# Kernel tuning notes

Measured on AMD Instinct MI355X. Metric: run time of the kernel, lower is better.

## Reference

```python
import jax, jax.numpy as jnp
import numpy as np

N = 8192          # number of nodes
A = 3             # number of adjacency relations
D_IN = 256
D_OUT = 64


def setup_inputs() -> dict:
    key = jax.random.key(0)
    k1, k2, k3, k4 = jax.random.split(key, 4)
    inputs = jax.random.normal(k1, (N, D_IN), dtype=jnp.float32)
    # dense adjacency stack [A, N, N] (weighted graph)
    adj_set = jax.random.uniform(k2, (A, N, N), dtype=jnp.float32)
    att = jax.random.uniform(k3, (A,), dtype=jnp.float32)
    w = jax.random.normal(k4, (D_IN, D_OUT), dtype=jnp.float32) * (1.0 / np.sqrt(D_IN))
    b = jnp.zeros((D_OUT,), dtype=jnp.float32)
    return {"inputs": inputs, "adj_set": adj_set, "att": att, "w": w, "b": b}


def reference(inputs, adj_set, att, w, b):
    # dropout=False -> identity; note: self.relu is never applied in forward
    support = jnp.matmul(inputs, w) + b                      # [N, D_OUT]
    # outputs = sum_i att[i] * (adj_i @ support), fused as one einsum
    outputs = jnp.einsum("a,anm,md->nd", att, adj_set, support)
    return outputs
```

## Files before the change

### kernel.cpp

```cpp
#include <hip/hip_runtime.h>
#include <hip/hip_bf16.h>


#define NNODES 8192
#define DIN    256
#define DOUT   64
#define NA     3
#define KSTACK (NA * NNODES)
#define KQ     (KSTACK / 4)
#define BK     256
#define NCH    (KQ / BK)
#define NSTRIP (NNODES / 64)

typedef float f32x4 __attribute__((ext_vector_type(4)));
typedef short s16x8 __attribute__((ext_vector_type(8)));

__device__ __forceinline__ unsigned short f2bf(float f) {
    __hip_bfloat16 h = __float2bfloat16(f);
    return __builtin_bit_cast(unsigned short, h);
}

__device__ __forceinline__ s16x8 pack8(f32x4 a, f32x4 b) {
    s16x8 o;
    o[0] = (short)f2bf(a[0]); o[1] = (short)f2bf(a[1]);
    o[2] = (short)f2bf(a[2]); o[3] = (short)f2bf(a[3]);
    o[4] = (short)f2bf(b[0]); o[5] = (short)f2bf(b[1]);
    o[6] = (short)f2bf(b[2]); o[7] = (short)f2bf(b[3]);
    return o;
}

__device__ __forceinline__ void gload_lds16(const float* g, float* l) {
    __builtin_amdgcn_global_load_lds(
        (const __attribute__((address_space(1))) void*)g,
        (__attribute__((address_space(3))) void*)l, 16, 0, 2);
}

__global__ __launch_bounds__(256) void zero_out(float* __restrict__ out) {
    f32x4 z = {0.f, 0.f, 0.f, 0.f};
    ((f32x4*)out)[(blockIdx.x << 8) + threadIdx.x] = z;
}

__global__ __launch_bounds__(256) void prep_support(
    const float* __restrict__ x, const float* __restrict__ w,
    const float* __restrict__ bias, const float* __restrict__ att,
    unsigned short* __restrict__ Bp)
{
    const int t = threadIdx.x;
    const int d = t & 63;
    const int m = (blockIdx.x << 2) + (t >> 6);

    const float* xr = x + (size_t)m * DIN;
    float acc = bias[d];
#pragma unroll 4
    for (int k = 0; k < DIN; k += 4) {
        f32x4 xv = *(const f32x4*)(xr + k);
        acc += xv[0] * w[(k + 0) * DOUT + d];
        acc += xv[1] * w[(k + 1) * DOUT + d];
        acc += xv[2] * w[(k + 2) * DOUT + d];
        acc += xv[3] * w[(k + 3) * DOUT + d];
    }

    const int kt   = m >> 5;
    const int kl   = m & 31;
    const int lane = ((kl >> 3) << 4) | (d & 15);
    const int j    = kl & 7;
    const int nt   = d >> 4;

    const size_t base    = (size_t)(kt * 4 + nt) * 512 + lane * 8 + j;
    const size_t aStride = (size_t)(NNODES / 32) * 4 * 512;

    const float a0 = att[0], a1 = att[1], a2 = att[2];
    Bp[base]               = f2bf(a0 * acc);
    Bp[base + aStride]     = f2bf(a1 * acc);
    Bp[base + 2 * aStride] = f2bf(a2 * acc);
}

__global__ __launch_bounds__(256, 2) void graphconv_gemm(
    const float* __restrict__ adj, const unsigned short* __restrict__ Bp,
    float* __restrict__ out)
{
    __shared__ float ldsf[16384];

    const int tid  = threadIdx.x;
    const int wv   = tid >> 6;
    const int lane = tid & 63;
    const int r    = lane & 15;
    const int g    = lane >> 4;
    const int r7   = r & 7;
    const int q     = blockIdx.x & 3;
    const int strip = blockIdx.x >> 2;
    const int row0  = strip * 64 + wv * 16;

    float* wbuf = &ldsf[wv << 12];

    f32x4 acc0 = {0.f, 0.f, 0.f, 0.f};
    f32x4 acc1 = {0.f, 0.f, 0.f, 0.f};
    f32x4 acc2 = {0.f, 0.f, 0.f, 0.f};
    f32x4 acc3 = {0.f, 0.f, 0.f, 0.f};

    const int c0 = (wv * 6 + strip) % NCH;

    for (int i = 0; i < NCH; ++i) {
        int c = c0 + i; if (c >= NCH) c -= NCH;
        const int k0 = q * KQ + c * BK;
        const float* ab = adj + ((size_t)(k0 >> 13) << 26) + (k0 & 8191);

#pragma unroll
        for (int p = 0; p < 16; ++p) {
            const float* gp = ab + (size_t)(row0 + p) * NNODES
                                 + ((lane ^ (p & 7)) << 2);
            gload_lds16(gp, wbuf + (p << 8));
        }
        asm volatile("s_waitcnt vmcnt(0)" ::: "memory");
        __builtin_amdgcn_sched_barrier(0);

        const s16x8* bp = (const s16x8*)Bp + ((size_t)(k0 >> 5) << 8) + lane;
        const float* lrow = wbuf + (r << 8);
#pragma unroll
        for (int t = 0; t < 8; ++t) {
            f32x4 v0 = *(const f32x4*)(lrow + ((t * 8 + ((2 * g) ^ r7)) << 2));
            f32x4 v1 = *(const f32x4*)(lrow + ((t * 8 + ((2 * g + 1) ^ r7)) << 2));
            s16x8 af = pack8(v0, v1);
            s16x8 b0 = bp[0];
            s16x8 b1 = bp[64];
            s16x8 b2 = bp[128];
            s16x8 b3 = bp[192];
            acc0 = __builtin_amdgcn_mfma_f32_16x16x32_bf16(af, b0, acc0, 0, 0, 0);
            acc1 = __builtin_amdgcn_mfma_f32_16x16x32_bf16(af, b1, acc1, 0, 0, 0);
            acc2 = __builtin_amdgcn_mfma_f32_16x16x32_bf16(af, b2, acc2, 0, 0, 0);
            acc3 = __builtin_amdgcn_mfma_f32_16x16x32_bf16(af, b3, acc3, 0, 0, 0);
            bp += 256;
        }
    }

    float* op = out + (size_t)row0 * DOUT;
#pragma unroll
    for (int j = 0; j < 4; ++j) {
        float* rp = op + (size_t)(4 * g + j) * DOUT + r;
        atomicAdd(rp,      acc0[j]);
        atomicAdd(rp + 16, acc1[j]);
        atomicAdd(rp + 32, acc2[j]);
        atomicAdd(rp + 48, acc3[j]);
    }
}

extern "C" void kernel_launch(void* const* d_in, const int* in_sizes, int n_in,
                              void* d_out, int out_size, void* d_ws, size_t ws_size,
                              hipStream_t stream) {
    const float* x   = (const float*)d_in[0];
    const float* adj = (const float*)d_in[1];
    const float* att = (const float*)d_in[2];
    const float* w   = (const float*)d_in[3];
    const float* b   = (const float*)d_in[4];
    float* out = (float*)d_out;
    unsigned short* Bp = (unsigned short*)d_ws;

    zero_out<<<NNODES * DOUT / 1024, 256, 0, stream>>>(out);
    prep_support<<<NNODES / 4, 256, 0, stream>>>(x, w, b, att, Bp);
    graphconv_gemm<<<NSTRIP * 4, 256, 0, stream>>>(adj, Bp, out);
}
```

Before: 186.4 us.

## Double-buffer per-wave adjacency staging and prefetch B fragments into registers

Each wave now owns two LDS buffers and issues the global-to-LDS loads for the next adjacency chunk before computing on the current one, waiting only on the older loads. All 32 B fragments for a chunk are loaded into registers up front instead of being interleaved with the MFMAs. LDS use doubles and launch bounds drop to one block per CU. This trades occupancy for explicit load/compute overlap.

```diff
diff --git a/kernel.cpp b/kernel.cpp
--- a/kernel.cpp
+++ b/kernel.cpp
@@ -75,11 +75,23 @@
     Bp[base + 2 * aStride] = f2bf(a2 * acc);
 }
 
-__global__ __launch_bounds__(256, 2) void graphconv_gemm(
+__device__ __forceinline__ void stage_chunk(
+    const float* __restrict__ adj, int row0, int k0, float* bufbase, int lane)
+{
+    const float* ab = adj + ((size_t)(k0 >> 13) << 26) + (k0 & 8191);
+#pragma unroll
+    for (int p = 0; p < 16; ++p) {
+        const float* gp = ab + (size_t)(row0 + p) * NNODES
+                             + ((lane ^ (p & 7)) << 2);
+        gload_lds16(gp, bufbase + (p << 8));
+    }
+}
+
+__global__ __launch_bounds__(256, 1) void graphconv_gemm(
     const float* __restrict__ adj, const unsigned short* __restrict__ Bp,
     float* __restrict__ out)
 {
-    __shared__ float ldsf[16384];
+    __shared__ float ldsf[32768];
 
     const int tid  = threadIdx.x;
     const int wv   = tid >> 6;
@@ -91,7 +103,7 @@
     const int strip = blockIdx.x >> 2;
     const int row0  = strip * 64 + wv * 16;
 
-    float* wbuf = &ldsf[wv << 12];
+    float* wbase = &ldsf[wv << 13];
 
     f32x4 acc0 = {0.f, 0.f, 0.f, 0.f};
     f32x4 acc1 = {0.f, 0.f, 0.f, 0.f};
@@ -100,36 +112,46 @@
 
     const int c0 = (wv * 6 + strip) % NCH;
 
+    stage_chunk(adj, row0, q * KQ + c0 * BK, wbase, lane);
+
     for (int i = 0; i < NCH; ++i) {
         int c = c0 + i; if (c >= NCH) c -= NCH;
-        const int k0 = q * KQ + c * BK;
-        const float* ab = adj + ((size_t)(k0 >> 13) << 26) + (k0 & 8191);
+        const int k0  = q * KQ + c * BK;
+        const int cur = i & 1;
 
+        const s16x8* __restrict__ bp =
+            (const s16x8*)Bp + ((size_t)(k0 >> 5) << 8) + lane;
+        s16x8 bq[32];
 #pragma unroll
-        for (int p = 0; p < 16; ++p) {
-            const float* gp = ab + (size_t)(row0 + p) * NNODES
-                                 + ((lane ^ (p & 7)) << 2);
-            gload_lds16(gp, wbuf + (p << 8));
-        }
-        asm volatile("s_waitcnt vmcnt(0)" ::: "memory");
+        for (int t = 0; t < 8; ++t)
+#pragma unroll
+            for (int n = 0; n < 4; ++n)
+                bq[t * 4 + n] = bp[t * 256 + n * 64];
+
         __builtin_amdgcn_sched_barrier(0);
 
-        const s16x8* bp = (const s16x8*)Bp + ((size_t)(k0 >> 5) << 8) + lane;
-        const float* lrow = wbuf + (r << 8);
+        const bool more = (i + 1 < NCH);
+        if (more) {
+            int cn = c + 1; if (cn >= NCH) cn = 0;
+            stage_chunk(adj, row0, q * KQ + cn * BK, wbase + ((cur ^ 1) << 12), lane);
+            asm volatile("s_waitcnt vmcnt(16)" ::: "memory");
+        } else {
+            asm volatile("s_waitcnt vmcnt(0)" ::: "memory");
+        }
+        __builtin_amdgcn_sched_barrier(0);
+
+        const float* lrow = wbase + (cur << 12) + (r << 8);
 #pragma unroll
         for (int t = 0; t < 8; ++t) {
-            f32x4 v0 = *(const f32x4*)(lrow + ((t * 8 + ((2 * g) ^ r7)) << 2));
-            f32x4 v1 = *(const f32x4*)(lrow + ((t * 8 + ((2 * g + 1) ^ r7)) << 2));
+            const int s0 = ((t << 3) + 2 * g)     ^ r7;
+            const int s1 = ((t << 3) + 2 * g + 1) ^ r7;
+            f32x4 v0 = *(const f32x4*)(lrow + (s0 << 2));
+            f32x4 v1 = *(const f32x4*)(lrow + (s1 << 2));
             s16x8 af = pack8(v0, v1);
-            s16x8 b0 = bp[0];
-            s16x8 b1 = bp[64];
-            s16x8 b2 = bp[128];
-            s16x8 b3 = bp[192];
-            acc0 = __builtin_amdgcn_mfma_f32_16x16x32_bf16(af, b0, acc0, 0, 0, 0);
-            acc1 = __builtin_amdgcn_mfma_f32_16x16x32_bf16(af, b1, acc1, 0, 0, 0);
-            acc2 = __builtin_amdgcn_mfma_f32_16x16x32_bf16(af, b2, acc2, 0, 0, 0);
-            acc3 = __builtin_amdgcn_mfma_f32_16x16x32_bf16(af, b3, acc3, 0, 0, 0);
-            bp += 256;
+            acc0 = __builtin_amdgcn_mfma_f32_16x16x32_bf16(af, bq[t*4+0], acc0, 0, 0, 0);
+            acc1 = __builtin_amdgcn_mfma_f32_16x16x32_bf16(af, bq[t*4+1], acc1, 0, 0, 0);
+            acc2 = __builtin_amdgcn_mfma_f32_16x16x32_bf16(af, bq[t*4+2], acc2, 0, 0, 0);
+            acc3 = __builtin_amdgcn_mfma_f32_16x16x32_bf16(af, bq[t*4+3], acc3, 0, 0, 0);
         }
     }
 
```

Result: slower. 194.4 us (+4.2%).
